# Kernel tuning notes

Measured on AMD Instinct MI355X. Metric: run time of the kernel, lower is better.

The kernel has to match this reference:

```python
import jax, jax.numpy as jnp
import numpy as np

H = 16  # n_heads
LN_EPS = 1e-5

def _ln(x, g, b):
    m = jnp.mean(x, axis=-1, keepdims=True)
    v = jnp.mean(jnp.square(x - m), axis=-1, keepdims=True)
    return (x - m) * jax.lax.rsqrt(v + LN_EPS) * g + b

def setup_inputs() -> dict:
    key = jax.random.key(0)
    ks = jax.random.split(key, 12)
    Nq, Nk, D = 4096, 4096, 1024
    s = 1.0 / np.sqrt(D)
    return {
        "query": jax.random.normal(ks[0], (Nq, D), jnp.float32),
        "key_": jax.random.normal(ks[1], (Nk, D), jnp.float32),
        "Wq": jax.random.uniform(ks[2], (D, D), jnp.float32, -s, s),
        "bq": jax.random.uniform(ks[3], (D,), jnp.float32, -s, s),
        "Wk": jax.random.uniform(ks[4], (D, D), jnp.float32, -s, s),
        "bk": jax.random.uniform(ks[5], (D,), jnp.float32, -s, s),
        "Wv": jax.random.uniform(ks[6], (D, D), jnp.float32, -s, s),
        "bv": jax.random.uniform(ks[7], (D,), jnp.float32, -s, s),
        "g1": jnp.ones((D,), jnp.float32),
        "b1": jnp.zeros((D,), jnp.float32),
        "Wl": jax.random.uniform(ks[8], (D, D), jnp.float32, -s, s),
        "bl": jax.random.uniform(ks[9], (D,), jnp.float32, -s, s),
        "g2": jnp.ones((D,), jnp.float32),
        "b2": jnp.zeros((D,), jnp.float32),
    }

def reference(query, key_, Wq, bq, Wk, bk, Wv, bv, g1, b1, Wl, bl, g2, b2):
    Nq, D = query.shape
    Nk = key_.shape[0]
    dh = D // H
    scale = 1.0 / jnp.sqrt(jnp.asarray(D, query.dtype))  # NOTE: full dim_V, not per-head
    Q = (query @ Wq + bq).reshape(Nq, H, dh)   # [Nq,H,dh]
    K = (key_ @ Wk + bk).reshape(Nk, H, dh)    # [Nk,H,dh]
    V = (key_ @ Wv + bv).reshape(Nk, H, dh)    # [Nk,H,dh]
    A = jax.nn.softmax(jnp.einsum('qhd,khd->hqk', Q, K) * scale, axis=-1)  # [H,Nq,Nk]
    O = Q + jnp.einsum('hqk,khd->qhd', A, V)   # residual on projected Q
    out = _ln(O.reshape(Nq, D), g1, b1)
    out = out + jax.nn.relu(out @ Wl + bl)
    return _ln(out, g2, b2)
```

## Files before the change

kernel.cpp:

```cpp
#include <hip/hip_runtime.h>
#include <hip/hip_bf16.h>
#include <stdint.h>

typedef __attribute__((ext_vector_type(4))) float  f32x4;
typedef __attribute__((ext_vector_type(8))) short  bf16x8;
typedef __attribute__((ext_vector_type(4))) float  float4v;
typedef __attribute__((ext_vector_type(4))) unsigned short u16x4;
typedef __attribute__((ext_vector_type(4))) uint32_t u32x4;

typedef uint32_t u32_as1 __attribute__((address_space(1)));
typedef uint32_t u32_as3 __attribute__((address_space(3)));

#define CEXP_SCALE 0.045084221f
#define INV_CEXP   22.180710f

__device__ __forceinline__ void gload_lds16(const void* g, void* l) {
  __builtin_amdgcn_global_load_lds((const u32_as1*)g, (u32_as3*)l, 16, 0, 0);
}

__device__ __forceinline__ unsigned short f2bf(float f) {
  union { float f; uint32_t u; } v; v.f = f;
  uint32_t r = v.u + 0x7fffu + ((v.u >> 16) & 1u);
  return (unsigned short)(r >> 16);
}
__device__ __forceinline__ float bf2f(unsigned short u) {
  union { uint32_t u; float f; } v; v.u = ((uint32_t)u) << 16;
  return v.f;
}
__device__ __forceinline__ uint32_t cvtpk_bf16(float lo, float hi) {
  uint32_t d;
  asm("v_cvt_pk_bf16_f32 %0, %1, %2" : "=v"(d) : "v"(lo), "v"(hi));
  return d;
}
__device__ __forceinline__ float exp2_hw(float x) {
  float r;
  asm("v_exp_f32 %0, %1" : "=v"(r) : "v"(x));
  return r;
}

__global__ __launch_bounds__(256) void wtrans4(const float* __restrict__ W0,
                                               const float* __restrict__ W1,
                                               const float* __restrict__ W2,
                                               const float* __restrict__ W3,
                                               unsigned short* __restrict__ WT, int D) {
  __shared__ float tile[32][33];
  const float* W = (blockIdx.z == 0) ? W0 : (blockIdx.z == 1) ? W1 : (blockIdx.z == 2) ? W2 : W3;
  unsigned short* WTz = WT + (size_t)blockIdx.z * D * D;
  int r0 = blockIdx.x * 32;
  int c0 = blockIdx.y * 32;
  int tc = threadIdx.x & 31;
  int tr = (threadIdx.x >> 5) * 4;
#pragma unroll
  for (int i = 0; i < 4; i++)
    tile[tr + i][tc] = W[(size_t)(r0 + tr + i) * D + c0 + tc];
  __syncthreads();
#pragma unroll
  for (int i = 0; i < 4; i++)
    WTz[(size_t)(c0 + tr + i) * D + r0 + tc] = f2bf(tile[tc][tr + i]);
}

template <int AF32>
__device__ __forceinline__ void gemm_core(
    const void* __restrict__ Ain, const unsigned short* __restrict__ BT,
    const float* __restrict__ bias, const float* __restrict__ bias2,
    unsigned short* __restrict__ C, unsigned short* __restrict__ VtOut,
    const unsigned short* __restrict__ RES,
    int M, int K, int relu_res, float cscale, int bm, int bn,
    unsigned char* AsmRaw, unsigned short* Bsm) {
  int tid = threadIdx.x;
  int lane = tid & 63;
  int w = tid >> 6;
  int wr = (w >> 1) * 64;
  int wc = (w & 1) * 64;
  int r = lane & 15;
  int q4 = lane >> 4;

  f32x4 acc[4][4] = {};

  for (int k0 = 0; k0 < K; k0 += 64) {
    if (AF32) {
      const float* Af = (const float*)Ain;
#pragma unroll
      for (int i = 0; i < 8; i++) {
        int idx = i * 256 + tid;
        int row = idx >> 4;
        int cg = (idx & 15) ^ (row & 15);
        gload_lds16(Af + (size_t)(bm + row) * K + k0 + cg * 4,
                    (float*)AsmRaw + idx * 4);
      }
    } else {
      const unsigned short* Ab = (const unsigned short*)Ain;
#pragma unroll
      for (int i = 0; i < 4; i++) {
        int idx = i * 256 + tid;
        int row = idx >> 3;
        int g = ((idx & 7) ^ (row & 7)) * 8;
        gload_lds16(Ab + (size_t)(bm + row) * K + k0 + g,
                    (unsigned short*)AsmRaw + idx * 8);
      }
    }
#pragma unroll
    for (int i = 0; i < 4; i++) {
      int idx = i * 256 + tid;
      int row = idx >> 3;
      int g = ((idx & 7) ^ (row & 7)) * 8;
      gload_lds16(BT + (size_t)(bn + row) * K + k0 + g, &Bsm[idx * 8]);
    }
    __syncthreads();
#pragma unroll
    for (int kk = 0; kk < 2; kk++) {
      bf16x8 af[4], bfr[4];
      if (AF32) {
        const float* AsF = (const float*)AsmRaw;
        int c0 = kk * 8 + q4 * 2;
#pragma unroll
        for (int mb = 0; mb < 4; mb++) {
          int row = wr + mb * 16 + r;
          const float* rp = AsF + row * 64;
          int x = row & 15;
          f32x4 a0 = *(const f32x4*)(rp + ((c0 ^ x) * 4));
          f32x4 a1 = *(const f32x4*)(rp + (((c0 + 1) ^ x) * 4));
          u32x4 t = {cvtpk_bf16(a0.x, a0.y), cvtpk_bf16(a0.z, a0.w),
                     cvtpk_bf16(a1.x, a1.y), cvtpk_bf16(a1.z, a1.w)};
          af[mb] = __builtin_bit_cast(bf16x8, t);
        }
      } else {
        const unsigned short* AsB = (const unsigned short*)AsmRaw;
        int ch = ((kk * 4 + q4) ^ (r & 7)) * 8;
#pragma unroll
        for (int mb = 0; mb < 4; mb++)
          af[mb] = *(const bf16x8*)&AsB[(wr + mb * 16 + r) * 64 + ch];
      }
      int chb = ((kk * 4 + q4) ^ (r & 7)) * 8;
#pragma unroll
      for (int nb = 0; nb < 4; nb++)
        bfr[nb] = *(const bf16x8*)&Bsm[(wc + nb * 16 + r) * 64 + chb];
#pragma unroll
      for (int mb = 0; mb < 4; mb++)
#pragma unroll
        for (int nb = 0; nb < 4; nb++)
          acc[mb][nb] = __builtin_amdgcn_mfma_f32_16x16x32_bf16(af[mb], bfr[nb], acc[mb][nb], 0, 0, 0);
    }
    __syncthreads();
  }

#pragma unroll
  for (int mb = 0; mb < 4; mb++) {
#pragma unroll
    for (int nb = 0; nb < 4; nb++) {
      int col = bn + wc + nb * 16 + r;
      bool second = (VtOut != nullptr) && (col >= 1024);
      int ccol = second ? (col - 1024) : col;
      float bv = second ? bias2[ccol] : bias[ccol];
      if (second) {
        u16x4 ov;
#pragma unroll
        for (int rr = 0; rr < 4; rr++)
          ov[rr] = f2bf(acc[mb][nb][rr] + bv);
        int row0 = bm + wr + mb * 16 + q4 * 4;
        *(u16x4*)(VtOut + (size_t)ccol * M + row0) = ov;
      } else {
#pragma unroll
        for (int rr = 0; rr < 4; rr++) {
          int row = bm + wr + mb * 16 + q4 * 4 + rr;
          float v = acc[mb][nb][rr] + bv;
          if (relu_res) {
            float res = bf2f(RES[(size_t)row * 1024 + ccol]);
            v = res + (v > 0.f ? v : 0.f);
          }
          C[(size_t)row * 1024 + ccol] = f2bf(v * cscale);
        }
      }
    }
  }
}

__global__ __launch_bounds__(256) void proj_gemm(
    const float* __restrict__ query, const float* __restrict__ key_,
    const unsigned short* __restrict__ WqT, const unsigned short* __restrict__ WkvT,
    const float* __restrict__ bq, const float* __restrict__ bk, const float* __restrict__ bv,
    unsigned short* __restrict__ Qs, unsigned short* __restrict__ Kp,
    unsigned short* __restrict__ Vt, int Nq, int D) {
  __shared__ __align__(16) unsigned char AsmRaw[128 * 64 * 4];
  __shared__ __align__(16) unsigned short Bsm[128 * 64];
  int bid = blockIdx.x;
  if (bid < 256) {
    gemm_core<1>(query, WqT, bq, nullptr, Qs, nullptr, nullptr,
                 Nq, D, 0, CEXP_SCALE, (bid & 31) * 128, (bid >> 5) * 128, AsmRaw, Bsm);
  } else {
    int b = bid - 256;
    gemm_core<1>(key_, WkvT, bk, bv, Kp, Vt, nullptr,
                 Nq, D, 0, 1.0f, (b & 31) * 128, (b >> 5) * 128, AsmRaw, Bsm);
  }
}

__global__ __launch_bounds__(256) void ffn_gemm(
    const unsigned short* __restrict__ A, const unsigned short* __restrict__ WlT,
    const float* __restrict__ bl, unsigned short* __restrict__ C,
    const unsigned short* __restrict__ RES, int Nq, int D) {
  __shared__ __align__(16) unsigned char AsmRaw[128 * 64 * 2];
  __shared__ __align__(16) unsigned short Bsm[128 * 64];
  int bid = blockIdx.x;
  gemm_core<0>(A, WlT, bl, nullptr, C, nullptr, RES,
               Nq, D, 1, 1.0f, (bid & 31) * 128, (bid >> 5) * 128, AsmRaw, Bsm);
}

__global__ __launch_bounds__(256, 4) void attn_kernel(
    const unsigned short* __restrict__ Qs,
    const unsigned short* __restrict__ Kp,
    const unsigned short* __restrict__ Vt,
    unsigned short* __restrict__ Opart,
    float* __restrict__ Lpart,
    int Nq, int Nk) {
  __shared__ __align__(16) unsigned short Ksm[2][4096];
  __shared__ __align__(16) unsigned short Vsm[2][4096];
  const int Dm = 1024;
  int tid = threadIdx.x;
  int w = tid >> 6;
  int lane = tid & 63;
  int r = lane & 15;
  int q4 = lane >> 4;
  int bid = blockIdx.x;
  int vid = ((bid & 7) << 7) + (bid >> 3);
  int h = vid >> 6;
  int qw = ((vid >> 1) & 31) * 128 + w * 32;
  int z = vid & 1;
  int k_beg = z * (Nk >> 1);
  const int NT = Nk >> 7;

  const unsigned short* Kb = Kp + h * 64;
  const unsigned short* Vb = Vt + (size_t)h * 64 * Nk;

  int srcA = r + ((lane & 16) << 1);
  int srcB = srcA + 16;
  bool hi_cb = (lane & 32) != 0;

  bf16x8 qf[2][2];
#pragma unroll
  for (int mb = 0; mb < 2; mb++)
#pragma unroll
    for (int s = 0; s < 2; s++)
      qf[mb][s] = *(const bf16x8*)(Qs + (size_t)(qw + mb * 16 + r) * Dm + h * 64 + s * 32 + q4 * 8);

  bf16x8 ones;
#pragma unroll
  for (int i = 0; i < 8; i++) ones[i] = (short)0x3F80;

  const f32x4 czero = {0.f, 0.f, 0.f, 0.f};
  f32x4 acc[2][4] = {};
  f32x4 acc_s[2] = {};

  auto STAGE = [&](int nb, int key0) {
    if (w < 2) {
#pragma unroll
      for (int k = 0; k < 4; k++) {
        int j = w * 4 + k;
        int s = j >> 2, cb = j & 3;
        gload_lds16(Kb + (size_t)(key0 + cb * 16 + r) * Dm + s * 32 + q4 * 8,
                    &Ksm[nb][j * 512]);
      }
    } else {
#pragma unroll
      for (int k = 0; k < 4; k++) {
        int j = (w - 2) * 4 + k;
        int s = j >> 2, db = j & 3;
        gload_lds16(Vb + (size_t)(db * 16 + r) * Nk + key0 + s * 32 + q4 * 8,
                    &Vsm[nb][j * 512]);
      }
    }
  };

  STAGE(0, k_beg);
  __syncthreads();

  int cur = 0;
  for (int t = 0; t < NT; ++t) {
    if (t + 1 < NT) STAGE(cur ^ 1, k_beg + (t + 1) * 64);

    bf16x8 kfr0[4], kfr1[4];
#pragma unroll
    for (int cb = 0; cb < 4; cb++) {
      kfr0[cb] = *(const bf16x8*)&Ksm[cur][(0 * 4 + cb) * 512 + lane * 8];
      kfr1[cb] = *(const bf16x8*)&Ksm[cur][(1 * 4 + cb) * 512 + lane * 8];
    }
    f32x4 sacc[2][4];
#pragma unroll
    for (int cb = 0; cb < 4; cb++)
#pragma unroll
      for (int mb = 0; mb < 2; mb++)
        sacc[mb][cb] = __builtin_amdgcn_mfma_f32_16x16x32_bf16(kfr0[cb], qf[mb][0], czero, 0, 0, 0);
#pragma unroll
    for (int cb = 0; cb < 4; cb++)
#pragma unroll
      for (int mb = 0; mb < 2; mb++)
        sacc[mb][cb] = __builtin_amdgcn_mfma_f32_16x16x32_bf16(kfr1[cb], qf[mb][1], sacc[mb][cb], 0, 0, 0);

    uint32_t pk[2][4][2];
#pragma unroll
    for (int mb = 0; mb < 2; mb++)
#pragma unroll
      for (int cb = 0; cb < 4; cb++) {
        float p0 = exp2_hw(sacc[mb][cb][0]);
        float p1 = exp2_hw(sacc[mb][cb][1]);
        float p2 = exp2_hw(sacc[mb][cb][2]);
        float p3 = exp2_hw(sacc[mb][cb][3]);
        pk[mb][cb][0] = cvtpk_bf16(p0, p1);
        pk[mb][cb][1] = cvtpk_bf16(p2, p3);
      }

#pragma unroll
    for (int s = 0; s < 2; s++) {
      bf16x8 pf[2];
#pragma unroll
      for (int mb = 0; mb < 2; mb++) {
        uint32_t s0 = hi_cb ? pk[mb][2 * s + 1][0] : pk[mb][2 * s][0];
        uint32_t s1 = hi_cb ? pk[mb][2 * s + 1][1] : pk[mb][2 * s][1];
        uint32_t w0 = (uint32_t)__shfl((int)s0, srcA);
        uint32_t w1 = (uint32_t)__shfl((int)s1, srcA);
        uint32_t w2 = (uint32_t)__shfl((int)s0, srcB);
        uint32_t w3 = (uint32_t)__shfl((int)s1, srcB);
        u32x4 tmp = {w0, w1, w2, w3};
        pf[mb] = __builtin_bit_cast(bf16x8, tmp);
      }
      acc_s[0] = __builtin_amdgcn_mfma_f32_16x16x32_bf16(pf[0], ones, acc_s[0], 0, 0, 0);
      acc_s[1] = __builtin_amdgcn_mfma_f32_16x16x32_bf16(pf[1], ones, acc_s[1], 0, 0, 0);
#pragma unroll
      for (int db = 0; db < 4; db++) {
        bf16x8 vfx = *(const bf16x8*)&Vsm[cur][(s * 4 + db) * 512 + lane * 8];
        acc[0][db] = __builtin_amdgcn_mfma_f32_16x16x32_bf16(pf[0], vfx, acc[0][db], 0, 0, 0);
        acc[1][db] = __builtin_amdgcn_mfma_f32_16x16x32_bf16(pf[1], vfx, acc[1][db], 0, 0, 0);
      }
    }

    __syncthreads();
    cur ^= 1;
  }

  unsigned short* Op = Opart + (size_t)z * Nq * Dm;
#pragma unroll
  for (int mb = 0; mb < 2; mb++)
#pragma unroll
    for (int rr = 0; rr < 4; rr++) {
      int qrow = qw + mb * 16 + q4 * 4 + rr;
      if (r == 0)
        Lpart[(size_t)(z * 16 + h) * Nq + qrow] = acc_s[mb][rr];
#pragma unroll
      for (int db = 0; db < 4; db++) {
        int col = h * 64 + db * 16 + r;
        Op[(size_t)qrow * Dm + col] = f2bf(acc[mb][db][rr]);
      }
    }
}

__global__ __launch_bounds__(256) void combine_ln(
    const unsigned short* __restrict__ Qs,
    const unsigned short* __restrict__ Op,
    const float* __restrict__ Lp,
    const float* __restrict__ g, const float* __restrict__ b,
    unsigned short* __restrict__ out, int Nq) {
  int row = blockIdx.x;
  int tid = threadIdx.x;
  int h = tid >> 4;
  size_t base = (size_t)row * 1024 + tid * 4;
  float linv = 1.0f / (Lp[(size_t)h * Nq + row] + Lp[(size_t)(16 + h) * Nq + row]);
  u16x4 qv = *(const u16x4*)(Qs + base);
  u16x4 a0 = *(const u16x4*)(Op + base);
  u16x4 a1 = *(const u16x4*)(Op + (size_t)Nq * 1024 + base);
  float x0 = bf2f(qv.x) * INV_CEXP + (bf2f(a0.x) + bf2f(a1.x)) * linv;
  float x1 = bf2f(qv.y) * INV_CEXP + (bf2f(a0.y) + bf2f(a1.y)) * linv;
  float x2 = bf2f(qv.z) * INV_CEXP + (bf2f(a0.z) + bf2f(a1.z)) * linv;
  float x3 = bf2f(qv.w) * INV_CEXP + (bf2f(a0.w) + bf2f(a1.w)) * linv;
  float s = x0 + x1 + x2 + x3;
  float s2 = x0 * x0 + x1 * x1 + x2 * x2 + x3 * x3;
#pragma unroll
  for (int m = 1; m < 64; m <<= 1) { s += __shfl_xor(s, m); s2 += __shfl_xor(s2, m); }
  __shared__ float red[8];
  int w = tid >> 6, lane = tid & 63;
  if (lane == 0) { red[w] = s; red[4 + w] = s2; }
  __syncthreads();
  s = red[0] + red[1] + red[2] + red[3];
  s2 = red[4] + red[5] + red[6] + red[7];
  float mean = s * (1.0f / 1024.0f);
  float var = s2 * (1.0f / 1024.0f) - mean * mean;
  float inv = rsqrtf(var + 1e-5f);
  float y0 = (x0 - mean) * inv * g[tid * 4 + 0] + b[tid * 4 + 0];
  float y1 = (x1 - mean) * inv * g[tid * 4 + 1] + b[tid * 4 + 1];
  float y2 = (x2 - mean) * inv * g[tid * 4 + 2] + b[tid * 4 + 2];
  float y3 = (x3 - mean) * inv * g[tid * 4 + 3] + b[tid * 4 + 3];
  u16x4 o = {f2bf(y0), f2bf(y1), f2bf(y2), f2bf(y3)};
  *(u16x4*)(out + base) = o;
}

template <int OUTF32>
__global__ __launch_bounds__(256) void ln_kernel(
    const unsigned short* __restrict__ X,
    const float* __restrict__ g, const float* __restrict__ b,
    void* __restrict__ outp, int D) {
  int row = blockIdx.x;
  int tid = threadIdx.x;
  const unsigned short* xr = X + (size_t)row * D;
  u16x4 xv = *(const u16x4*)(xr + tid * 4);
  float x0 = bf2f(xv.x), x1 = bf2f(xv.y), x2 = bf2f(xv.z), x3 = bf2f(xv.w);
  float s = x0 + x1 + x2 + x3;
  float s2 = x0 * x0 + x1 * x1 + x2 * x2 + x3 * x3;
#pragma unroll
  for (int m = 1; m < 64; m <<= 1) { s += __shfl_xor(s, m); s2 += __shfl_xor(s2, m); }
  __shared__ float red[8];
  int w = tid >> 6, lane = tid & 63;
  if (lane == 0) { red[w] = s; red[4 + w] = s2; }
  __syncthreads();
  s = red[0] + red[1] + red[2] + red[3];
  s2 = red[4] + red[5] + red[6] + red[7];
  float mean = s * (1.0f / 1024.0f);
  float var = s2 * (1.0f / 1024.0f) - mean * mean;
  float inv = rsqrtf(var + 1e-5f);
  float y0 = (x0 - mean) * inv * g[tid * 4 + 0] + b[tid * 4 + 0];
  float y1 = (x1 - mean) * inv * g[tid * 4 + 1] + b[tid * 4 + 1];
  float y2 = (x2 - mean) * inv * g[tid * 4 + 2] + b[tid * 4 + 2];
  float y3 = (x3 - mean) * inv * g[tid * 4 + 3] + b[tid * 4 + 3];
  if (OUTF32) {
    float4v o = {y0, y1, y2, y3};
    *(float4v*)((float*)outp + (size_t)row * D + tid * 4) = o;
  } else {
    u16x4 o = {f2bf(y0), f2bf(y1), f2bf(y2), f2bf(y3)};
    *(u16x4*)((unsigned short*)outp + (size_t)row * D + tid * 4) = o;
  }
}

extern "C" void kernel_launch(void* const* d_in, const int* in_sizes, int n_in,
                              void* d_out, int out_size, void* d_ws, size_t ws_size,
                              hipStream_t stream) {
  (void)in_sizes; (void)n_in; (void)out_size; (void)ws_size;
  const float* query = (const float*)d_in[0];
  const float* key_  = (const float*)d_in[1];
  const float* Wq = (const float*)d_in[2];
  const float* bq = (const float*)d_in[3];
  const float* Wk = (const float*)d_in[4];
  const float* bk = (const float*)d_in[5];
  const float* Wv = (const float*)d_in[6];
  const float* bv_ = (const float*)d_in[7];
  const float* g1 = (const float*)d_in[8];
  const float* b1 = (const float*)d_in[9];
  const float* Wl = (const float*)d_in[10];
  const float* bl = (const float*)d_in[11];
  const float* g2 = (const float*)d_in[12];
  const float* b2 = (const float*)d_in[13];
  float* out = (float*)d_out;

  const int Nq = 4096, Nk = 4096, D = 1024;
  const size_t MEl = (size_t)4096 * 1024;

  unsigned short* w16 = (unsigned short*)d_ws;
  unsigned short* WqT = w16;
  unsigned short* WkT = WqT + (size_t)D * D;
  unsigned short* WvT = WkT + (size_t)D * D;
  unsigned short* WlT = WvT + (size_t)D * D;
  unsigned short* Qs  = w16 + 4 * (size_t)D * D;
  unsigned short* Kp  = Qs + MEl;
  unsigned short* Vt  = Kp + MEl;
  unsigned short* Opart = Vt + MEl;
  unsigned short* out1  = Opart + 2 * MEl;
  float* Lpart = (float*)(out1 + MEl);
  unsigned short* out2  = Opart;

  wtrans4<<<dim3(32, 32, 4), 256, 0, stream>>>(Wq, Wk, Wv, Wl, WqT, D);

  proj_gemm<<<768, 256, 0, stream>>>(query, key_, WqT, WkT, bq, bk, bv_,
                                     Qs, Kp, Vt, Nq, D);

  attn_kernel<<<1024, 256, 0, stream>>>(Qs, Kp, Vt, Opart, Lpart, Nq, Nk);

  combine_ln<<<4096, 256, 0, stream>>>(Qs, Opart, Lpart, g1, b1, out1, Nq);
  ffn_gemm<<<256, 256, 0, stream>>>(out1, WlT, bl, out2, out1, Nq, D);
  ln_kernel<1><<<4096, 256, 0, stream>>>(out2, g2, b2, (void*)out, D);
}
```

Measured before the change: 173.2 us.

## Split attention keys four ways when workspace allows and raise MFMA wave priority

The attention kernel is templated on the number of key splits. When the workspace is large enough it uses four splits (2048 blocks) instead of two, and the combine kernel sums that many partial outputs and row sums. s_setprio is also raised around the MFMA sections so matrix work gets issued ahead of other waves. More splits give more blocks and better occupancy across the CUs, at the cost of extra partial-output traffic and more work in the combine step.

```diff
diff --git a/kernel.cpp b/kernel.cpp
--- a/kernel.cpp
+++ b/kernel.cpp
@@ -205,6 +205,7 @@
                Nq, D, 1, 1.0f, (bid & 31) * 128, (bid >> 5) * 128, AsmRaw, Bsm);
 }
 
+template <int NZ>
 __global__ __launch_bounds__(256, 4) void attn_kernel(
     const unsigned short* __restrict__ Qs,
     const unsigned short* __restrict__ Kp,
@@ -221,12 +222,13 @@
   int r = lane & 15;
   int q4 = lane >> 4;
   int bid = blockIdx.x;
-  int vid = ((bid & 7) << 7) + (bid >> 3);
-  int h = vid >> 6;
-  int qw = ((vid >> 1) & 31) * 128 + w * 32;
-  int z = vid & 1;
-  int k_beg = z * (Nk >> 1);
-  const int NT = Nk >> 7;
+  int vid = (bid & 7) * (64 * NZ) + (bid >> 3);
+  int h = vid / (32 * NZ);
+  int rem = vid - h * (32 * NZ);
+  int qw = (rem / NZ) * 128 + w * 32;
+  int z = rem % NZ;
+  int k_beg = z * (Nk / NZ);
+  const int NT = (Nk / NZ) >> 6;
 
   const unsigned short* Kb = Kp + h * 64;
   const unsigned short* Vb = Vt + (size_t)h * 64 * Nk;
@@ -284,6 +286,7 @@
       kfr1[cb] = *(const bf16x8*)&Ksm[cur][(1 * 4 + cb) * 512 + lane * 8];
     }
     f32x4 sacc[2][4];
+    __builtin_amdgcn_s_setprio(1);
 #pragma unroll
     for (int cb = 0; cb < 4; cb++)
 #pragma unroll
@@ -294,6 +297,7 @@
 #pragma unroll
       for (int mb = 0; mb < 2; mb++)
         sacc[mb][cb] = __builtin_amdgcn_mfma_f32_16x16x32_bf16(kfr1[cb], qf[mb][1], sacc[mb][cb], 0, 0, 0);
+    __builtin_amdgcn_s_setprio(0);
 
     uint32_t pk[2][4][2];
 #pragma unroll
@@ -322,6 +326,7 @@
         u32x4 tmp = {w0, w1, w2, w3};
         pf[mb] = __builtin_bit_cast(bf16x8, tmp);
       }
+      __builtin_amdgcn_s_setprio(1);
       acc_s[0] = __builtin_amdgcn_mfma_f32_16x16x32_bf16(pf[0], ones, acc_s[0], 0, 0, 0);
       acc_s[1] = __builtin_amdgcn_mfma_f32_16x16x32_bf16(pf[1], ones, acc_s[1], 0, 0, 0);
 #pragma unroll
@@ -330,6 +335,7 @@
         acc[0][db] = __builtin_amdgcn_mfma_f32_16x16x32_bf16(pf[0], vfx, acc[0][db], 0, 0, 0);
         acc[1][db] = __builtin_amdgcn_mfma_f32_16x16x32_bf16(pf[1], vfx, acc[1][db], 0, 0, 0);
       }
+      __builtin_amdgcn_s_setprio(0);
     }
 
     __syncthreads();
@@ -352,6 +358,7 @@
     }
 }
 
+template <int NZ>
 __global__ __launch_bounds__(256) void combine_ln(
     const unsigned short* __restrict__ Qs,
     const unsigned short* __restrict__ Op,
@@ -362,14 +369,21 @@
   int tid = threadIdx.x;
   int h = tid >> 4;
   size_t base = (size_t)row * 1024 + tid * 4;
-  float linv = 1.0f / (Lp[(size_t)h * Nq + row] + Lp[(size_t)(16 + h) * Nq + row]);
+  float lsum = 0.f;
+#pragma unroll
+  for (int zz = 0; zz < NZ; zz++) lsum += Lp[(size_t)(zz * 16 + h) * Nq + row];
+  float linv = 1.0f / lsum;
   u16x4 qv = *(const u16x4*)(Qs + base);
-  u16x4 a0 = *(const u16x4*)(Op + base);
-  u16x4 a1 = *(const u16x4*)(Op + (size_t)Nq * 1024 + base);
-  float x0 = bf2f(qv.x) * INV_CEXP + (bf2f(a0.x) + bf2f(a1.x)) * linv;
-  float x1 = bf2f(qv.y) * INV_CEXP + (bf2f(a0.y) + bf2f(a1.y)) * linv;
-  float x2 = bf2f(qv.z) * INV_CEXP + (bf2f(a0.z) + bf2f(a1.z)) * linv;
-  float x3 = bf2f(qv.w) * INV_CEXP + (bf2f(a0.w) + bf2f(a1.w)) * linv;
+  float ax = 0.f, ay = 0.f, az = 0.f, aw = 0.f;
+#pragma unroll
+  for (int zz = 0; zz < NZ; zz++) {
+    u16x4 av = *(const u16x4*)(Op + (size_t)zz * Nq * 1024 + base);
+    ax += bf2f(av.x); ay += bf2f(av.y); az += bf2f(av.z); aw += bf2f(av.w);
+  }
+  float x0 = bf2f(qv.x) * INV_CEXP + ax * linv;
+  float x1 = bf2f(qv.y) * INV_CEXP + ay * linv;
+  float x2 = bf2f(qv.z) * INV_CEXP + az * linv;
+  float x3 = bf2f(qv.w) * INV_CEXP + aw * linv;
   float s = x0 + x1 + x2 + x3;
   float s2 = x0 * x0 + x1 * x1 + x2 * x2 + x3 * x3;
 #pragma unroll
@@ -430,7 +444,7 @@
 extern "C" void kernel_launch(void* const* d_in, const int* in_sizes, int n_in,
                               void* d_out, int out_size, void* d_ws, size_t ws_size,
                               hipStream_t stream) {
-  (void)in_sizes; (void)n_in; (void)out_size; (void)ws_size;
+  (void)in_sizes; (void)n_in; (void)out_size;
   const float* query = (const float*)d_in[0];
   const float* key_  = (const float*)d_in[1];
   const float* Wq = (const float*)d_in[2];
@@ -449,17 +463,20 @@
 
   const int Nq = 4096, Nk = 4096, D = 1024;
   const size_t MEl = (size_t)4096 * 1024;
+  const size_t DD = (size_t)D * D;
+
+  const int NZ = (ws_size >= 2 * (4 * DD + 4 * MEl + 4 * MEl) + 4ull * 4 * 16 * Nq + (1u << 20)) ? 4 : 2;
 
   unsigned short* w16 = (unsigned short*)d_ws;
   unsigned short* WqT = w16;
-  unsigned short* WkT = WqT + (size_t)D * D;
-  unsigned short* WvT = WkT + (size_t)D * D;
-  unsigned short* WlT = WvT + (size_t)D * D;
-  unsigned short* Qs  = w16 + 4 * (size_t)D * D;
+  unsigned short* WkT = WqT + DD;
+  unsigned short* WvT = WkT + DD;
+  unsigned short* WlT = WvT + DD;
+  unsigned short* Qs  = w16 + 4 * DD;
   unsigned short* Kp  = Qs + MEl;
   unsigned short* Vt  = Kp + MEl;
   unsigned short* Opart = Vt + MEl;
-  unsigned short* out1  = Opart + 2 * MEl;
+  unsigned short* out1  = Opart + (size_t)NZ * MEl;
   float* Lpart = (float*)(out1 + MEl);
   unsigned short* out2  = Opart;
 
@@ -468,9 +485,13 @@
   proj_gemm<<<768, 256, 0, stream>>>(query, key_, WqT, WkT, bq, bk, bv_,
                                      Qs, Kp, Vt, Nq, D);
 
-  attn_kernel<<<1024, 256, 0, stream>>>(Qs, Kp, Vt, Opart, Lpart, Nq, Nk);
-
-  combine_ln<<<4096, 256, 0, stream>>>(Qs, Opart, Lpart, g1, b1, out1, Nq);
+  if (NZ == 4) {
+    attn_kernel<4><<<2048, 256, 0, stream>>>(Qs, Kp, Vt, Opart, Lpart, Nq, Nk);
+    combine_ln<4><<<4096, 256, 0, stream>>>(Qs, Opart, Lpart, g1, b1, out1, Nq);
+  } else {
+    attn_kernel<2><<<1024, 256, 0, stream>>>(Qs, Kp, Vt, Opart, Lpart, Nq, Nk);
+    combine_ln<2><<<4096, 256, 0, stream>>>(Qs, Opart, Lpart, g1, b1, out1, Nq);
+  }
   ffn_gemm<<<256, 256, 0, stream>>>(out1, WlT, bl, out2, out1, Nq, D);
   ln_kernel<1><<<4096, 256, 0, stream>>>(out2, g2, b2, (void*)out, D);
 }
```

Measured after the change: 178.9 us. 3.3% more time.
